# Optimization experiments

Measured on AMD Instinct MI355X. Metric: run time of the kernel, lower is better.

The kernel has to match this reference:

```python
import jax, jax.numpy as jnp
import numpy as np

N_NODES = 1024; DEG = 24; K_NN = 12
C_S = 384; C_Z = 128; C_G = 16; N_RBF = 64
N_EDGES = N_NODES * DEG          # 24576
N_EE = N_EDGES * K_NN            # 294912 edge-edge pairs
LN_EPS = 1e-5
RBF_MIN, RBF_MAX = 0.0, 20.0


def _layernorm(x, w, b):
    m = x.mean(-1, keepdims=True)
    v = ((x - m) ** 2).mean(-1, keepdims=True)
    return (x - m) * jax.lax.rsqrt(v + LN_EPS) * w + b


def setup_inputs() -> dict:
    key = jax.random.key(0)
    ks = iter(jax.random.split(key, 40))

    def lin(i, o):
        w = jax.random.normal(next(ks), (i, o), jnp.float32) / np.sqrt(i)
        b = jax.random.normal(next(ks), (o,), jnp.float32) * 0.01
        return w, b

    node_features = jax.random.normal(next(ks), (N_NODES, C_S), jnp.float32)
    node_trans = jax.random.normal(next(ks), (N_NODES, 3), jnp.float32) * 10.0
    edge_features = jax.random.normal(next(ks), (N_EDGES, C_Z), jnp.float32)

    # edge_index sorted by destination (column 1), fixed in-degree DEG per node
    rng = np.random.default_rng(0)
    dst = np.repeat(np.arange(N_NODES), DEG)
    src = rng.integers(0, N_NODES, size=N_EDGES)
    edge_index = jnp.asarray(np.stack([src, dst]), jnp.int32)

    # edge-edge kNN graph: each edge paired with K_NN other edges sharing the
    # same destination node (mirrors knn_graph(..., batch=sorted_edge_index[1]))
    t = np.arange(N_EDGES)
    base = (t // DEG) * DEG
    off = t % DEG
    nbr = base[:, None] + (off[:, None] + 1 + np.arange(K_NN)[None, :]) % DEG  # [E,K]
    edge_edge_index = jnp.asarray(
        np.stack([nbr.reshape(-1), np.repeat(t, K_NN)]), jnp.int32)  # [2, N_EE]

    ln_w = jnp.ones((C_Z,), jnp.float32); ln_b = jnp.zeros((C_Z,), jnp.float32)
    wl_w, wl_b = lin(C_S, C_G)
    wr_w, wr_b = lin(C_S, C_G)
    ep_w, ep_b = lin(C_Z, C_Z)
    eg_w, eg_b = lin(C_Z, C_Z)
    dg_w, dg_b = lin(C_G * C_G, C_Z)
    dp_w, dp_b = lin(N_RBF, C_Z)
    lno_w = jnp.ones((C_Z,), jnp.float32); lno_b = jnp.zeros((C_Z,), jnp.float32)
    lo_w, lo_b = lin(C_Z, C_Z)
    og_w, og_b = lin(C_Z, C_Z)

    return dict(node_features=node_features, node_trans=node_trans,
                edge_features=edge_features,
                ln_w=ln_w, ln_b=ln_b, wl_w=wl_w, wl_b=wl_b, wr_w=wr_w, wr_b=wr_b,
                ep_w=ep_w, ep_b=ep_b, eg_w=eg_w, eg_b=eg_b,
                dg_w=dg_w, dg_b=dg_b, dp_w=dp_w, dp_b=dp_b,
                lno_w=lno_w, lno_b=lno_b, lo_w=lo_w, lo_b=lo_b,
                og_w=og_w, og_b=og_b,
                edge_index=edge_index, edge_edge_index=edge_edge_index)


def reference(node_features, node_trans, edge_features,
              ln_w, ln_b, wl_w, wl_b, wr_w, wr_b,
              ep_w, ep_b, eg_w, eg_b, dg_w, dg_b, dp_w, dp_b,
              lno_w, lno_b, lo_w, lo_b, og_w, og_b,
              edge_index, edge_edge_index):
    eps = 1e-8
    src = edge_index[0]
    eei0, eei1 = edge_edge_index[0], edge_edge_index[1]
    n1 = src[eei1]  # source node of target edge of each pair
    n2 = src[eei0]  # source node of source edge of each pair

    ef = _layernorm(edge_features, ln_w, ln_b)            # [E, c_z]
    nl = node_features @ wl_w + wl_b                      # [N, c_g]
    nr = node_features @ wr_w + wr_b                      # [N, c_g]

    # per-pair outer product, flattened: [N_EE, c_g*c_g]
    e3 = (nl[n1][:, :, None] * nr[n2][:, None, :]).reshape(-1, C_G * C_G)
    gate3 = e3 @ dg_w + dg_b                              # [N_EE, c_z]

    d = jnp.linalg.norm(node_trans[n1] - node_trans[n2] + eps, axis=-1)
    mu = jnp.linspace(RBF_MIN, RBF_MAX, N_RBF)
    sigma = (RBF_MAX - RBF_MIN) / N_RBF
    rbf = jnp.exp(-(((d[:, None] - mu) / sigma) ** 2))    # [N_EE, num_rbf]
    e3f = jax.nn.sigmoid(gate3) * (rbf @ dp_w + dp_b)

    e2 = jax.nn.sigmoid(ef @ eg_w + eg_b) * (ef @ ep_w + ep_b)  # [E, c_z]
    upd = e2[eei0] * e3f                                  # [N_EE, c_z]
    upd = jax.ops.segment_sum(upd, eei0, num_segments=N_EDGES)  # [E, c_z]

    upd = _layernorm(upd, lno_w, lno_b) @ lo_w + lo_b
    upd = upd * jax.nn.sigmoid(ef @ og_w + og_b)
    return upd
```

## Files before the change

kernel.cpp:

```cpp
#include <hip/hip_runtime.h>
#include <math.h>

#define N_NODES 1024
#define DEG     24
#define K_NN    12
#define C_S     384
#define C_Z     128
#define C_G     16
#define N_RBF   64
#define N_EDGES (N_NODES*DEG)

typedef short short8 __attribute__((ext_vector_type(8)));
typedef float f32x4  __attribute__((ext_vector_type(4)));

__device__ __forceinline__ float sigf(float x) {
  return __builtin_amdgcn_rcpf(1.f + __expf(-x));
}

__device__ __forceinline__ short f2b(float x) {
  union { float f; unsigned u; } v; v.f = x;
  unsigned r = v.u + 0x7FFFu + ((v.u >> 16) & 1u);
  return (short)(r >> 16);
}
__device__ __forceinline__ float b2f(short s) {
  union { unsigned u; float f; } v; v.u = ((unsigned)(unsigned short)s) << 16;
  return v.f;
}

__global__ __launch_bounds__(256) void k_prep(
    const float* __restrict__ nf, const float* __restrict__ wl_w, const float* __restrict__ wl_b,
    const float* __restrict__ wr_w, const float* __restrict__ wr_b,
    const float* __restrict__ dg_w,
    const float* __restrict__ eg, const float* __restrict__ ep,
    const float* __restrict__ og, const float* __restrict__ lo,
    const float* __restrict__ dp_w,
    short* __restrict__ nlB, short* __restrict__ At,
    short* __restrict__ wT, short* __restrict__ dpT)
{
  __shared__ float rows[4][C_S];
  __shared__ float nrv[4][C_G];
  __shared__ float tb[32][33];
  int b = blockIdx.x, t = threadIdx.x;
  if (b < 256) {
    for (int v = t; v < 4*C_S; v += 256) rows[v/C_S][v%C_S] = nf[(size_t)b*4*C_S + v];
    __syncthreads();
    {
      int nd = t >> 6, lt = t & 63;
      int c = lt >> 1, jseg = lt & 1, cc = c & 15;
      const float* w = (c < 16) ? wl_w : wr_w;
      float acc = 0.f;
      #pragma unroll 8
      for (int j = jseg*192; j < jseg*192 + 192; ++j) acc += rows[nd][j] * w[j*C_G + cc];
      acc += __shfl_xor(acc, 1);
      if (jseg == 0) {
        float v = acc + ((c < 16) ? wl_b[cc] : wr_b[cc]);
        if (c < 16) nlB[(b*4 + nd)*C_G + cc] = f2b(v);
        else nrv[nd][cc] = v;
      }
    }
    __syncthreads();
    {
      int c2 = t & 127, ih = t >> 7;
      float a4[4][8];
      #pragma unroll
      for (int nd = 0; nd < 4; ++nd)
        #pragma unroll
        for (int q = 0; q < 8; ++q) a4[nd][q] = 0.f;
      for (int j = 0; j < C_G; ++j) {
        float w8[8];
        #pragma unroll
        for (int q = 0; q < 8; ++q) w8[q] = dg_w[(size_t)((ih*8 + q)*C_G + j)*C_Z + c2];
        #pragma unroll
        for (int nd = 0; nd < 4; ++nd) {
          float nv = nrv[nd][j];
          #pragma unroll
          for (int q = 0; q < 8; ++q) a4[nd][q] += nv * w8[q];
        }
      }
      #pragma unroll
      for (int nd = 0; nd < 4; ++nd) {
        short8 o8;
        #pragma unroll
        for (int q = 0; q < 8; ++q) o8[q] = f2b(a4[nd][q]);
        *(short8*)&At[(size_t)(b*4 + nd)*2048 + c2*16 + ih*8] = o8;
      }
    }
    return;
  }
  if (b < 320) {
    int bb = b - 256;
    int w = bb >> 4, tile = bb & 15, bi = tile >> 2, bj = tile & 3;
    const float* src = (w == 0) ? eg : (w == 1) ? ep : (w == 2) ? og : lo;
    short* dst = wT + w * 16384;
    int c = t & 31, r0 = t >> 5;
    #pragma unroll
    for (int p = 0; p < 4; ++p) { int r = r0 + p*8; tb[r][c] = src[(bi*32 + r)*128 + bj*32 + c]; }
    __syncthreads();
    #pragma unroll
    for (int p = 0; p < 4; ++p) { int r = r0 + p*8; dst[(bj*32 + r)*128 + bi*32 + c] = f2b(tb[c][r]); }
    return;
  }
  {
    int c2 = t & 127, rh = t >> 7;
    for (int r = rh*36; r < rh*36 + 36; ++r)
      dpT[c2*72 + r] = (r < 64) ? f2b(dp_w[r*128 + c2]) : (short)0;
  }
}

__global__ __launch_bounds__(256) void k_gates2(
    const float* __restrict__ efin, const float* __restrict__ ln_w, const float* __restrict__ ln_b,
    const short* __restrict__ wT,
    const float* __restrict__ eg_b, const float* __restrict__ ep_b, const float* __restrict__ og_b,
    float* __restrict__ e2, short* __restrict__ ogs)
{
  __shared__ short xn[16*136];
  int t = threadIdx.x;
  int ebase = blockIdx.x * 16;
  {
    int el = t >> 4, sub = t & 15, c0 = sub*8;
    float x[8];
    size_t ein = (size_t)(ebase + el) * C_Z + c0;
    float4 v0 = *(const float4*)(efin + ein);
    float4 v1 = *(const float4*)(efin + ein + 4);
    x[0]=v0.x; x[1]=v0.y; x[2]=v0.z; x[3]=v0.w;
    x[4]=v1.x; x[5]=v1.y; x[6]=v1.z; x[7]=v1.w;
    float s = 0.f;
    #pragma unroll
    for (int q = 0; q < 8; ++q) s += x[q];
    s += __shfl_xor(s,1); s += __shfl_xor(s,2); s += __shfl_xor(s,4); s += __shfl_xor(s,8);
    float mean = s * (1.f/128.f);
    float vs = 0.f;
    #pragma unroll
    for (int q = 0; q < 8; ++q) { float d = x[q]-mean; vs += d*d; }
    vs += __shfl_xor(vs,1); vs += __shfl_xor(vs,2); vs += __shfl_xor(vs,4); vs += __shfl_xor(vs,8);
    float rstd = rsqrtf(vs*(1.f/128.f) + 1e-5f);
    short8 o;
    #pragma unroll
    for (int q = 0; q < 8; ++q)
      o[q] = f2b((x[q]-mean)*rstd*ln_w[c0+q] + ln_b[c0+q]);
    *(short8*)&xn[el*136 + c0] = o;
  }
  __syncthreads();
  int wv = t >> 6, lane = t & 63, col = lane & 15, grp = lane >> 4;
  short8 a[4];
  #pragma unroll
  for (int ks = 0; ks < 4; ++ks)
    a[ks] = *(const short8*)&xn[col*136 + ks*32 + grp*8];
  #pragma unroll
  for (int hh = 0; hh < 2; ++hh) {
    int ch = col + 16*(wv*2 + hh);
    f32x4 aE = (f32x4){0.f,0.f,0.f,0.f}, aP = aE, aO = aE;
    #pragma unroll
    for (int ks = 0; ks < 4; ++ks) {
      aE = __builtin_amdgcn_mfma_f32_16x16x32_bf16(
          a[ks], *(const short8*)(wT + (size_t)ch*128 + ks*32 + grp*8), aE, 0, 0, 0);
      aP = __builtin_amdgcn_mfma_f32_16x16x32_bf16(
          a[ks], *(const short8*)(wT + 16384 + (size_t)ch*128 + ks*32 + grp*8), aP, 0, 0, 0);
      aO = __builtin_amdgcn_mfma_f32_16x16x32_bf16(
          a[ks], *(const short8*)(wT + 32768 + (size_t)ch*128 + ks*32 + grp*8), aO, 0, 0, 0);
    }
    float egb = eg_b[ch], epb = ep_b[ch], ogb = og_b[ch];
    #pragma unroll
    for (int r = 0; r < 4; ++r) {
      size_t e = (size_t)(ebase + grp*4 + r);
      e2[e*C_Z + ch]  = sigf(aE[r] + egb) * (aP[r] + epb);
      ogs[e*C_Z + ch] = f2b(sigf(aO[r] + ogb));
    }
  }
}

__global__ __launch_bounds__(512) void k_pairsout(
    const int* __restrict__ eidx, const float* __restrict__ pos,
    const short* __restrict__ nlB, const short* __restrict__ At, const short* __restrict__ dpTg,
    const float* __restrict__ dg_b, const float* __restrict__ dp_b,
    const float* __restrict__ e2, const float* __restrict__ lno_w, const float* __restrict__ lno_b,
    const short* __restrict__ wTlo, const float* __restrict__ lo_b, const short* __restrict__ ogs,
    float* __restrict__ out)
{
  __shared__ float p4[DEG][4];
  __shared__ int   s24[DEG];
  __shared__ short nlb[DEG*C_G];
  __shared__ short UnL[8][138];
  int t = threadIdx.x;
  int g = blockIdx.x / 3, sub = blockIdx.x - g*3;
  if (t < DEG) {
    int s = eidx[g*DEG + t];
    s24[t] = s;
    p4[t][0] = pos[s*3+0]; p4[t][1] = pos[s*3+1]; p4[t][2] = pos[s*3+2]; p4[t][3] = 0.f;
  }
  __syncthreads();
  for (int v = t; v < DEG*C_G; v += 512)
    nlb[v] = nlB[s24[v>>4]*C_G + (v & 15)];
  __syncthreads();

  int wv = t >> 6, lane = t & 63, col = lane & 15, grp = lane >> 4;
  int o = sub*8 + wv;
  size_t e = (size_t)g*DEG + o;

  {
    float dgb[8], dpb[8];
    #pragma unroll
    for (int q = 0; q < 8; ++q) { int c = col+16*q; dgb[q] = dg_b[c]; dpb[q] = dp_b[c]; }
    const float RS = 3.2f, MUS = 20.f/63.f;

    int n2 = s24[o];
    int o2 = o - 1 - col; if (o2 < 0) o2 += DEG;
    bool vk = (col < K_NN);
    float d;
    {
      float dx = p4[o2][0]-p4[o][0]+1e-8f;
      float dy = p4[o2][1]-p4[o][1]+1e-8f;
      float dz = p4[o2][2]-p4[o][2]+1e-8f;
      d = vk ? sqrtf(dx*dx+dy*dy+dz*dz) : 1.0e6f;
    }
    short8 zz = {0,0,0,0,0,0,0,0};
    short8 a_nl = zz;
    if (vk && grp < 2) a_nl = *(const short8*)&nlb[o2*C_G + grp*8];
    short8 a_r0, a_r1;
    #pragma unroll
    for (int j = 0; j < 8; ++j) {
      float z0 = (d - (float)(grp*8 + j)*MUS)*RS;
      float z1 = (d - (float)(32 + grp*8 + j)*MUS)*RS;
      a_r0[j] = f2b(__expf(-z0*z0));
      a_r1[j] = f2b(__expf(-z1*z1));
    }
    const short8* Ab = (const short8*)(At + (size_t)n2*2048);
    float v1 = 0.f, v2 = 0.f;
    #pragma unroll
    for (int cb = 0; cb < 8; ++cb) {
      f32x4 accg = (f32x4){dgb[cb],dgb[cb],dgb[cb],dgb[cb]};
      f32x4 accd = (f32x4){dpb[cb],dpb[cb],dpb[cb],dpb[cb]};
      short8 b = (grp < 2) ? Ab[(col+16*cb)*2 + grp] : zz;
      accg = __builtin_amdgcn_mfma_f32_16x16x32_bf16(a_nl, b, accg, 0, 0, 0);
      const short* dbase = dpTg + (col+16*cb)*72 + grp*8;
      accd = __builtin_amdgcn_mfma_f32_16x16x32_bf16(a_r0, *(const short8*)dbase,      accd, 0, 0, 0);
      accd = __builtin_amdgcn_mfma_f32_16x16x32_bf16(a_r1, *(const short8*)(dbase+32), accd, 0, 0, 0);
      float sacc = 0.f;
      #pragma unroll
      for (int r = 0; r < 4; ++r)
        sacc += sigf(accg[r]) * accd[r];
      sacc = (grp == 3) ? 0.f : sacc;
      sacc += __shfl_xor(sacc, 16); sacc += __shfl_xor(sacc, 32);
      v1 = (cb == grp)     ? sacc : v1;
      v2 = (cb == grp + 4) ? sacc : v2;
    }
    v1 *= e2[e*C_Z + lane];
    v2 *= e2[e*C_Z + 64 + lane];
    float s = v1 + v2;
    s += __shfl_xor(s,1); s += __shfl_xor(s,2); s += __shfl_xor(s,4);
    s += __shfl_xor(s,8); s += __shfl_xor(s,16); s += __shfl_xor(s,32);
    float mean = s * (1.f/128.f);
    float d1 = v1 - mean, d2 = v2 - mean;
    float vsum = d1*d1 + d2*d2;
    vsum += __shfl_xor(vsum,1); vsum += __shfl_xor(vsum,2); vsum += __shfl_xor(vsum,4);
    vsum += __shfl_xor(vsum,8); vsum += __shfl_xor(vsum,16); vsum += __shfl_xor(vsum,32);
    float rstd = rsqrtf(vsum*(1.f/128.f) + 1e-5f);
    UnL[wv][lane]      = f2b(d1*rstd*lno_w[lane]      + lno_b[lane]);
    UnL[wv][64 + lane] = f2b(d2*rstd*lno_w[64 + lane] + lno_b[64 + lane]);
  }
  __syncthreads();

  {
    short8 zz = {0,0,0,0,0,0,0,0};
    short8 ua[4];
    #pragma unroll
    for (int ks = 0; ks < 4; ++ks)
      ua[ks] = (col < 8) ? *(const short8*)&UnL[col][ks*32 + grp*8] : zz;
    int ch = col + 16*wv;
    f32x4 oacc = (f32x4){0.f,0.f,0.f,0.f};
    #pragma unroll
    for (int ks = 0; ks < 4; ++ks)
      oacc = __builtin_amdgcn_mfma_f32_16x16x32_bf16(
          ua[ks], *(const short8*)(wTlo + (size_t)ch*128 + ks*32 + grp*8), oacc, 0, 0, 0);
    if (grp < 2) {
      float lob = lo_b[ch];
      #pragma unroll
      for (int r = 0; r < 4; ++r) {
        size_t eo = (size_t)(g*DEG + sub*8 + grp*4 + r);
        out[eo*C_Z + ch] = (oacc[r] + lob) * b2f(ogs[eo*C_Z + ch]);
      }
    }
  }
}

extern "C" void kernel_launch(void* const* d_in, const int* in_sizes, int n_in,
                              void* d_out, int out_size, void* d_ws, size_t ws_size,
                              hipStream_t stream)
{
  const float* nf    = (const float*)d_in[0];
  const float* pos   = (const float*)d_in[1];
  const float* efin  = (const float*)d_in[2];
  const float* ln_w  = (const float*)d_in[3];
  const float* ln_b  = (const float*)d_in[4];
  const float* wl_w  = (const float*)d_in[5];
  const float* wl_b  = (const float*)d_in[6];
  const float* wr_w  = (const float*)d_in[7];
  const float* wr_b  = (const float*)d_in[8];
  const float* ep_w  = (const float*)d_in[9];
  const float* ep_b  = (const float*)d_in[10];
  const float* eg_w  = (const float*)d_in[11];
  const float* eg_b  = (const float*)d_in[12];
  const float* dg_w  = (const float*)d_in[13];
  const float* dg_b  = (const float*)d_in[14];
  const float* dp_w  = (const float*)d_in[15];
  const float* dp_b  = (const float*)d_in[16];
  const float* lno_w = (const float*)d_in[17];
  const float* lno_b = (const float*)d_in[18];
  const float* lo_w  = (const float*)d_in[19];
  const float* lo_b  = (const float*)d_in[20];
  const float* og_w  = (const float*)d_in[21];
  const float* og_b  = (const float*)d_in[22];
  const int*   eidx  = (const int*)d_in[23];

  float* ws   = (float*)d_ws;
  short* nlBw = (short*)(ws + 0);
  short* dpTw = (short*)(ws + 8192);
  short* wTw  = (short*)(ws + 16384);
  short* Atw  = (short*)(ws + 49152);
  float* e2w  = ws + 1097728;
  short* ogw  = (short*)(ws + 4243456);
  float* outp = (float*)d_out;

  k_prep    <<<321, 256, 0, stream>>>(nf, wl_w, wl_b, wr_w, wr_b, dg_w,
                                      eg_w, ep_w, og_w, lo_w, dp_w,
                                      nlBw, Atw, wTw, dpTw);
  k_gates2  <<<1536, 256, 0, stream>>>(efin, ln_w, ln_b, wTw, eg_b, ep_b, og_b, e2w, ogw);
  k_pairsout<<<3072, 512, 0, stream>>>(eidx, pos, nlBw, Atw, dpTw, dg_b, dp_b,
                                       e2w, lno_w, lno_b, wTw + 49152, lo_b, ogw, outp);
}
```

Before: 102.7 us.

## Split fused pair/output kernel into pair-reduction and full-tile output GEMM

Splits the fused pairs+output kernel in two. The first kernel computes the per-edge aggregated update and its layernorm using 256-thread blocks of 4 edges, and writes the bf16 normalized rows to a workspace buffer. The second kernel runs the final linear layer and output gate over full 16-edge MFMA tiles, removing the half-empty tiles of the old 8-edge version. This trades an extra kernel launch and a global round trip of the intermediate for better MFMA utilization and smaller blocks.

```diff
diff --git a/kernel.cpp b/kernel.cpp
--- a/kernel.cpp
+++ b/kernel.cpp
@@ -169,116 +169,116 @@
   }
 }
 
-__global__ __launch_bounds__(512) void k_pairsout(
+__global__ __launch_bounds__(256) void k_pairs2(
     const int* __restrict__ eidx, const float* __restrict__ pos,
     const short* __restrict__ nlB, const short* __restrict__ At, const short* __restrict__ dpTg,
     const float* __restrict__ dg_b, const float* __restrict__ dp_b,
     const float* __restrict__ e2, const float* __restrict__ lno_w, const float* __restrict__ lno_b,
-    const short* __restrict__ wTlo, const float* __restrict__ lo_b, const short* __restrict__ ogs,
-    float* __restrict__ out)
+    short* __restrict__ Un)
 {
   __shared__ float p4[DEG][4];
   __shared__ int   s24[DEG];
   __shared__ short nlb[DEG*C_G];
-  __shared__ short UnL[8][138];
   int t = threadIdx.x;
-  int g = blockIdx.x / 3, sub = blockIdx.x - g*3;
+  int g = blockIdx.x / 6, sub = blockIdx.x - g*6;
   if (t < DEG) {
     int s = eidx[g*DEG + t];
     s24[t] = s;
     p4[t][0] = pos[s*3+0]; p4[t][1] = pos[s*3+1]; p4[t][2] = pos[s*3+2]; p4[t][3] = 0.f;
   }
   __syncthreads();
-  for (int v = t; v < DEG*C_G; v += 512)
+  for (int v = t; v < DEG*C_G; v += 256)
     nlb[v] = nlB[s24[v>>4]*C_G + (v & 15)];
   __syncthreads();
 
   int wv = t >> 6, lane = t & 63, col = lane & 15, grp = lane >> 4;
-  int o = sub*8 + wv;
+  int o = sub*4 + wv;
   size_t e = (size_t)g*DEG + o;
 
+  float dgb[8], dpb[8];
+  #pragma unroll
+  for (int q = 0; q < 8; ++q) { int c = col+16*q; dgb[q] = dg_b[c]; dpb[q] = dp_b[c]; }
+  const float RS = 3.2f, MUS = 20.f/63.f;
+
+  int n2 = s24[o];
+  int o2 = o - 1 - col; if (o2 < 0) o2 += DEG;
+  bool vk = (col < K_NN);
+  float d;
   {
-    float dgb[8], dpb[8];
-    #pragma unroll
-    for (int q = 0; q < 8; ++q) { int c = col+16*q; dgb[q] = dg_b[c]; dpb[q] = dp_b[c]; }
-    const float RS = 3.2f, MUS = 20.f/63.f;
-
-    int n2 = s24[o];
-    int o2 = o - 1 - col; if (o2 < 0) o2 += DEG;
-    bool vk = (col < K_NN);
-    float d;
-    {
-      float dx = p4[o2][0]-p4[o][0]+1e-8f;
-      float dy = p4[o2][1]-p4[o][1]+1e-8f;
-      float dz = p4[o2][2]-p4[o][2]+1e-8f;
-      d = vk ? sqrtf(dx*dx+dy*dy+dz*dz) : 1.0e6f;
-    }
-    short8 zz = {0,0,0,0,0,0,0,0};
-    short8 a_nl = zz;
-    if (vk && grp < 2) a_nl = *(const short8*)&nlb[o2*C_G + grp*8];
-    short8 a_r0, a_r1;
-    #pragma unroll
-    for (int j = 0; j < 8; ++j) {
-      float z0 = (d - (float)(grp*8 + j)*MUS)*RS;
-      float z1 = (d - (float)(32 + grp*8 + j)*MUS)*RS;
-      a_r0[j] = f2b(__expf(-z0*z0));
-      a_r1[j] = f2b(__expf(-z1*z1));
-    }
-    const short8* Ab = (const short8*)(At + (size_t)n2*2048);
-    float v1 = 0.f, v2 = 0.f;
-    #pragma unroll
-    for (int cb = 0; cb < 8; ++cb) {
-      f32x4 accg = (f32x4){dgb[cb],dgb[cb],dgb[cb],dgb[cb]};
-      f32x4 accd = (f32x4){dpb[cb],dpb[cb],dpb[cb],dpb[cb]};
-      short8 b = (grp < 2) ? Ab[(col+16*cb)*2 + grp] : zz;
-      accg = __builtin_amdgcn_mfma_f32_16x16x32_bf16(a_nl, b, accg, 0, 0, 0);
-      const short* dbase = dpTg + (col+16*cb)*72 + grp*8;
-      accd = __builtin_amdgcn_mfma_f32_16x16x32_bf16(a_r0, *(const short8*)dbase,      accd, 0, 0, 0);
-      accd = __builtin_amdgcn_mfma_f32_16x16x32_bf16(a_r1, *(const short8*)(dbase+32), accd, 0, 0, 0);
-      float sacc = 0.f;
-      #pragma unroll
-      for (int r = 0; r < 4; ++r)
-        sacc += sigf(accg[r]) * accd[r];
-      sacc = (grp == 3) ? 0.f : sacc;
-      sacc += __shfl_xor(sacc, 16); sacc += __shfl_xor(sacc, 32);
-      v1 = (cb == grp)     ? sacc : v1;
-      v2 = (cb == grp + 4) ? sacc : v2;
-    }
-    v1 *= e2[e*C_Z + lane];
-    v2 *= e2[e*C_Z + 64 + lane];
-    float s = v1 + v2;
-    s += __shfl_xor(s,1); s += __shfl_xor(s,2); s += __shfl_xor(s,4);
-    s += __shfl_xor(s,8); s += __shfl_xor(s,16); s += __shfl_xor(s,32);
-    float mean = s * (1.f/128.f);
-    float d1 = v1 - mean, d2 = v2 - mean;
-    float vsum = d1*d1 + d2*d2;
-    vsum += __shfl_xor(vsum,1); vsum += __shfl_xor(vsum,2); vsum += __shfl_xor(vsum,4);
-    vsum += __shfl_xor(vsum,8); vsum += __shfl_xor(vsum,16); vsum += __shfl_xor(vsum,32);
-    float rstd = rsqrtf(vsum*(1.f/128.f) + 1e-5f);
-    UnL[wv][lane]      = f2b(d1*rstd*lno_w[lane]      + lno_b[lane]);
-    UnL[wv][64 + lane] = f2b(d2*rstd*lno_w[64 + lane] + lno_b[64 + lane]);
-  }
-  __syncthreads();
-
-  {
-    short8 zz = {0,0,0,0,0,0,0,0};
-    short8 ua[4];
-    #pragma unroll
-    for (int ks = 0; ks < 4; ++ks)
-      ua[ks] = (col < 8) ? *(const short8*)&UnL[col][ks*32 + grp*8] : zz;
-    int ch = col + 16*wv;
+    float dx = p4[o2][0]-p4[o][0]+1e-8f;
+    float dy = p4[o2][1]-p4[o][1]+1e-8f;
+    float dz = p4[o2][2]-p4[o][2]+1e-8f;
+    d = vk ? sqrtf(dx*dx+dy*dy+dz*dz) : 1.0e6f;
+  }
+  short8 zz = {0,0,0,0,0,0,0,0};
+  short8 a_nl = zz;
+  if (vk && grp < 2) a_nl = *(const short8*)&nlb[o2*C_G + grp*8];
+  short8 a_r0, a_r1;
+  #pragma unroll
+  for (int j = 0; j < 8; ++j) {
+    float z0 = (d - (float)(grp*8 + j)*MUS)*RS;
+    float z1 = (d - (float)(32 + grp*8 + j)*MUS)*RS;
+    a_r0[j] = f2b(__expf(-z0*z0));
+    a_r1[j] = f2b(__expf(-z1*z1));
+  }
+  const short8* Ab = (const short8*)(At + (size_t)n2*2048);
+  float v1 = 0.f, v2 = 0.f;
+  #pragma unroll
+  for (int cb = 0; cb < 8; ++cb) {
+    f32x4 accg = (f32x4){dgb[cb],dgb[cb],dgb[cb],dgb[cb]};
+    f32x4 accd = (f32x4){dpb[cb],dpb[cb],dpb[cb],dpb[cb]};
+    short8 b = (grp < 2) ? Ab[(col+16*cb)*2 + grp] : zz;
+    accg = __builtin_amdgcn_mfma_f32_16x16x32_bf16(a_nl, b, accg, 0, 0, 0);
+    const short* dbase = dpTg + (col+16*cb)*72 + grp*8;
+    accd = __builtin_amdgcn_mfma_f32_16x16x32_bf16(a_r0, *(const short8*)dbase,      accd, 0, 0, 0);
+    accd = __builtin_amdgcn_mfma_f32_16x16x32_bf16(a_r1, *(const short8*)(dbase+32), accd, 0, 0, 0);
+    float sacc = 0.f;
+    #pragma unroll
+    for (int r = 0; r < 4; ++r)
+      sacc += sigf(accg[r]) * accd[r];
+    sacc = (grp == 3) ? 0.f : sacc;
+    sacc += __shfl_xor(sacc, 16); sacc += __shfl_xor(sacc, 32);
+    v1 = (cb == grp)     ? sacc : v1;
+    v2 = (cb == grp + 4) ? sacc : v2;
+  }
+  v1 *= e2[e*C_Z + lane];
+  v2 *= e2[e*C_Z + 64 + lane];
+  float s = v1 + v2;
+  s += __shfl_xor(s,1); s += __shfl_xor(s,2); s += __shfl_xor(s,4);
+  s += __shfl_xor(s,8); s += __shfl_xor(s,16); s += __shfl_xor(s,32);
+  float mean = s * (1.f/128.f);
+  float d1 = v1 - mean, d2 = v2 - mean;
+  float vsum = d1*d1 + d2*d2;
+  vsum += __shfl_xor(vsum,1); vsum += __shfl_xor(vsum,2); vsum += __shfl_xor(vsum,4);
+  vsum += __shfl_xor(vsum,8); vsum += __shfl_xor(vsum,16); vsum += __shfl_xor(vsum,32);
+  float rstd = rsqrtf(vsum*(1.f/128.f) + 1e-5f);
+  Un[e*C_Z + lane]      = f2b(d1*rstd*lno_w[lane]      + lno_b[lane]);
+  Un[e*C_Z + 64 + lane] = f2b(d2*rstd*lno_w[64 + lane] + lno_b[64 + lane]);
+}
+
+__global__ __launch_bounds__(256) void k_out3(
+    const short* __restrict__ Un, const short* __restrict__ wTlo, const float* __restrict__ lo_b,
+    const short* __restrict__ ogs, float* __restrict__ out)
+{
+  int t = threadIdx.x, wv = t >> 6, lane = t & 63, col = lane & 15, grp = lane >> 4;
+  int ebase = blockIdx.x * 16;
+  short8 ua[4];
+  #pragma unroll
+  for (int ks = 0; ks < 4; ++ks)
+    ua[ks] = *(const short8*)(Un + (size_t)(ebase + col)*C_Z + ks*32 + grp*8);
+  #pragma unroll
+  for (int hh = 0; hh < 2; ++hh) {
+    int ch = col + 16*(wv*2 + hh);
     f32x4 oacc = (f32x4){0.f,0.f,0.f,0.f};
     #pragma unroll
     for (int ks = 0; ks < 4; ++ks)
       oacc = __builtin_amdgcn_mfma_f32_16x16x32_bf16(
           ua[ks], *(const short8*)(wTlo + (size_t)ch*128 + ks*32 + grp*8), oacc, 0, 0, 0);
-    if (grp < 2) {
-      float lob = lo_b[ch];
-      #pragma unroll
-      for (int r = 0; r < 4; ++r) {
-        size_t eo = (size_t)(g*DEG + sub*8 + grp*4 + r);
-        out[eo*C_Z + ch] = (oacc[r] + lob) * b2f(ogs[eo*C_Z + ch]);
-      }
+    float lob = lo_b[ch];
+    #pragma unroll
+    for (int r = 0; r < 4; ++r) {
+      size_t e = (size_t)(ebase + grp*4 + r);
+      out[e*C_Z + ch] = (oacc[r] + lob) * b2f(ogs[e*C_Z + ch]);
     }
   }
 }
@@ -319,12 +319,14 @@
   short* Atw  = (short*)(ws + 49152);
   float* e2w  = ws + 1097728;
   short* ogw  = (short*)(ws + 4243456);
+  short* Unw  = (short*)(ws + 5816320);
   float* outp = (float*)d_out;
 
-  k_prep    <<<321, 256, 0, stream>>>(nf, wl_w, wl_b, wr_w, wr_b, dg_w,
-                                      eg_w, ep_w, og_w, lo_w, dp_w,
-                                      nlBw, Atw, wTw, dpTw);
-  k_gates2  <<<1536, 256, 0, stream>>>(efin, ln_w, ln_b, wTw, eg_b, ep_b, og_b, e2w, ogw);
-  k_pairsout<<<3072, 512, 0, stream>>>(eidx, pos, nlBw, Atw, dpTw, dg_b, dp_b,
-                                       e2w, lno_w, lno_b, wTw + 49152, lo_b, ogw, outp);
-}
+  k_prep  <<<321, 256, 0, stream>>>(nf, wl_w, wl_b, wr_w, wr_b, dg_w,
+                                    eg_w, ep_w, og_w, lo_w, dp_w,
+                                    nlBw, Atw, wTw, dpTw);
+  k_gates2<<<1536, 256, 0, stream>>>(efin, ln_w, ln_b, wTw, eg_b, ep_b, og_b, e2w, ogw);
+  k_pairs2<<<6144, 256, 0, stream>>>(eidx, pos, nlBw, Atw, dpTw, dg_b, dp_b,
+                                     e2w, lno_w, lno_b, Unw);
+  k_out3  <<<1536, 256, 0, stream>>>(Unw, wTw + 49152, lo_b, ogw, outp);
+}
```

Measured after the change: 103.9 us. Within noise of the previous version (+1.2%).
